# Kernel optimization log

Measured on AMD Instinct MI355X. Metric: run time of the kernel, lower is better.

Reference implementation:

```python
import jax, jax.numpy as jnp
import numpy as np

N, E, C, O, H, W, K = 32, 512, 64, 128, 64, 64, 3


def setup_inputs() -> dict:
    key = jax.random.key(0)
    k1, k2, k3, k4, k5, k6 = jax.random.split(key, 6)
    scale_w = 1.0 / np.sqrt(E)
    return {
        "embedding": jax.random.normal(k1, (N, E), dtype=jnp.float32),
        "images": jax.random.normal(k2, (N, C, H, W), dtype=jnp.float32),
        "w_weight": jax.random.uniform(k3, (O * C * K * K, E), dtype=jnp.float32, minval=-scale_w, maxval=scale_w),
        "w_bias": jax.random.uniform(k4, (O * C * K * K,), dtype=jnp.float32, minval=-scale_w, maxval=scale_w),
        "b_weight": jax.random.uniform(k5, (O, E), dtype=jnp.float32, minval=-scale_w, maxval=scale_w),
        "b_bias": jax.random.uniform(k6, (O,), dtype=jnp.float32, minval=-scale_w, maxval=scale_w),
    }


def reference(embedding, images, w_weight, w_bias, b_weight, b_bias):
    n, c, h, w = images.shape
    o = b_bias.shape[0]
    # per-sample generated filters and biases
    c1_w = embedding @ w_weight.T + w_bias          # [N, O*C*K*K]
    c1_b = embedding @ b_weight.T + b_bias          # [N, O]
    filt = c1_w.reshape(n, o, c, K, K)              # matches torch view(O, C*K*K)
    # im2col equivalent: pad then gather 3x3 shifted views -> [N,C,K,K,H,W]
    xp = jnp.pad(images, ((0, 0), (0, 0), (1, 1), (1, 1)))
    patches = jnp.stack(
        [xp[:, :, i:i + h, j:j + w] for i in range(K) for j in range(K)], axis=2
    ).reshape(n, c, K, K, h, w)
    out = jnp.einsum('nocij,ncijhw->nohw', filt, patches)
    return out + c1_b[:, :, None, None]
```

## Files before the change

kernel.cpp:

```cpp
#include <hip/hip_runtime.h>
#include <hip/hip_bf16.h>

#define N_  32
#define E_  512
#define C_  64
#define O_  128
#define H_  64
#define W_  64
#define CK9 576
#define M_  (O_*CK9)

typedef __bf16 bf16x8 __attribute__((ext_vector_type(8)));
typedef __bf16 bf16x4 __attribute__((ext_vector_type(4)));
typedef float  f32x4  __attribute__((ext_vector_type(4)));

__global__ __launch_bounds__(256) void gen_filters(
    const float* __restrict__ emb, const float* __restrict__ w_weight,
    const float* __restrict__ w_bias, __bf16* __restrict__ filt)
{
    __shared__ __align__(16) __bf16 embS[32 * 520];
    __shared__ __align__(16) __bf16 wS[128 * 40];

    int tid  = threadIdx.x;
    int wave = tid >> 6, lane = tid & 63;
    int quad = lane >> 4, l16 = lane & 15;
    int m0 = blockIdx.x * 128;

#pragma unroll
    for (int i = 0; i < 16; i++) {
        int idx = (i * 256 + tid) * 4;
        int n = idx >> 9, e = idx & 511;
        f32x4 v = *reinterpret_cast<const f32x4*>(emb + n * 512 + e);
        bf16x4 b;
        b[0] = (__bf16)v[0]; b[1] = (__bf16)v[1]; b[2] = (__bf16)v[2]; b[3] = (__bf16)v[3];
        *reinterpret_cast<bf16x4*>(&embS[n * 520 + e]) = b;
    }

    f32x4 acc[2][2];
#pragma unroll
    for (int mi = 0; mi < 2; mi++)
#pragma unroll
        for (int ni = 0; ni < 2; ni++)
            acc[mi][ni] = (f32x4){0.f, 0.f, 0.f, 0.f};

    int sub = tid & 7, rbase = tid >> 3;

    for (int kk = 0; kk < 16; kk++) {
        int k0 = kk * 32;
        __syncthreads();
#pragma unroll
        for (int q = 0; q < 4; q++) {
            int row = rbase + q * 32;
            f32x4 v = *reinterpret_cast<const f32x4*>(
                w_weight + (size_t)(m0 + row) * 512 + k0 + sub * 4);
            bf16x4 b;
            b[0] = (__bf16)v[0]; b[1] = (__bf16)v[1]; b[2] = (__bf16)v[2]; b[3] = (__bf16)v[3];
            *reinterpret_cast<bf16x4*>(&wS[row * 40 + sub * 4]) = b;
        }
        __syncthreads();

        bf16x8 a0 = *reinterpret_cast<const bf16x8*>(&wS[(wave * 32 + l16) * 40 + quad * 8]);
        bf16x8 a1 = *reinterpret_cast<const bf16x8*>(&wS[(wave * 32 + 16 + l16) * 40 + quad * 8]);
        bf16x8 b0 = *reinterpret_cast<const bf16x8*>(&embS[l16 * 520 + k0 + quad * 8]);
        bf16x8 b1 = *reinterpret_cast<const bf16x8*>(&embS[(16 + l16) * 520 + k0 + quad * 8]);
        acc[0][0] = __builtin_amdgcn_mfma_f32_16x16x32_bf16(a0, b0, acc[0][0], 0, 0, 0);
        acc[0][1] = __builtin_amdgcn_mfma_f32_16x16x32_bf16(a0, b1, acc[0][1], 0, 0, 0);
        acc[1][0] = __builtin_amdgcn_mfma_f32_16x16x32_bf16(a1, b0, acc[1][0], 0, 0, 0);
        acc[1][1] = __builtin_amdgcn_mfma_f32_16x16x32_bf16(a1, b1, acc[1][1], 0, 0, 0);
    }

#pragma unroll
    for (int mi = 0; mi < 2; mi++) {
#pragma unroll
        for (int r = 0; r < 4; r++) {
            int m = m0 + wave * 32 + mi * 16 + quad * 4 + r;
            int o = m / 576;
            int rem = m - o * 576;
            int c = rem / 9;
            int t = rem - c * 9;
            size_t base = (size_t)o * 576 + t * 64 + c;
            float bias = w_bias[m];
#pragma unroll
            for (int ni = 0; ni < 2; ni++) {
                int n = ni * 16 + l16;
                filt[(size_t)n * M_ + base] = (__bf16)(acc[mi][ni][r] + bias);
            }
        }
    }
}

__global__ __launch_bounds__(256) void gen_bias(
    const float* __restrict__ emb, const float* __restrict__ b_weight,
    const float* __restrict__ b_bias, float* __restrict__ c1b)
{
    int wid  = (blockIdx.x * 256 + threadIdx.x) >> 6;
    int lane = threadIdx.x & 63;
    int n = wid >> 7, o = wid & 127;
    const float* e = emb + (size_t)n * E_ + lane * 8;
    const float* b = b_weight + (size_t)o * E_ + lane * 8;
    f32x4 e0 = *reinterpret_cast<const f32x4*>(e);
    f32x4 e1 = *reinterpret_cast<const f32x4*>(e + 4);
    f32x4 w0 = *reinterpret_cast<const f32x4*>(b);
    f32x4 w1 = *reinterpret_cast<const f32x4*>(b + 4);
    float s = e0[0]*w0[0] + e0[1]*w0[1] + e0[2]*w0[2] + e0[3]*w0[3]
            + e1[0]*w1[0] + e1[1]*w1[1] + e1[2]*w1[2] + e1[3]*w1[3];
#pragma unroll
    for (int off = 32; off; off >>= 1) s += __shfl_xor(s, off, 64);
    if (lane == 0) c1b[wid] = s + b_bias[o];
}

__global__ __launch_bounds__(256) void conv_gemm(
    const float* __restrict__ img, const __bf16* __restrict__ filt,
    const float* __restrict__ c1b, float* __restrict__ out)
{
    __shared__ __align__(16) __bf16 slab[4 * 66 * 72];

    int tid  = threadIdx.x;
    int wave = tid >> 6, lane = tid & 63;
    int quad = lane >> 4, l16 = lane & 15;

    int blk = blockIdx.x;
    int n     = ((blk & 7) << 2) + ((blk >> 3) & 3);
    int strip = blk >> 5;

    const float* imgn = img + (size_t)n * (C_ * H_ * W_);
    const __bf16* fBase = filt + (size_t)n * M_ + (size_t)(wave * 32 + l16) * CK9 + quad * 8;

    for (int pt2 = 0; pt2 < 2; pt2++) {
        int pt = strip * 2 + pt2;
        int h0 = pt * 2;

        __syncthreads();

#pragma unroll
        for (int i = 0; i < 16; i++) {
            int idx = i * 256 + tid;
            int wq  = (idx & 15) * 4;
            int rc  = idx >> 4;
            int r = rc >> 6, c = rc & 63;
            int hh = h0 - 1 + r;
            f32x4 v = {0.f, 0.f, 0.f, 0.f};
            if ((unsigned)hh < 64u)
                v = *reinterpret_cast<const f32x4*>(imgn + ((size_t)c << 12) + (hh << 6) + wq);
            __bf16* d = &slab[(r * 66 + wq + 1) * 72 + c];
            d[0]   = (__bf16)v[0];
            d[72]  = (__bf16)v[1];
            d[144] = (__bf16)v[2];
            d[216] = (__bf16)v[3];
        }
#pragma unroll
        for (int idx = tid; idx < 512; idx += 256) {
            int cc = idx & 63, rj = idx >> 6;
            int r = rj >> 1, col = (rj & 1) * 65;
            slab[(r * 66 + col) * 72 + cc] = (__bf16)0.f;
        }
        __syncthreads();

        f32x4 acc[2][8];
#pragma unroll
        for (int mi = 0; mi < 2; mi++)
#pragma unroll
            for (int ni = 0; ni < 8; ni++)
                acc[mi][ni] = (f32x4){0.f, 0.f, 0.f, 0.f};

#pragma unroll
        for (int kh = 0; kh < 2; kh++) {
            bf16x8 aR[2][9];
#pragma unroll
            for (int mi = 0; mi < 2; mi++)
#pragma unroll
                for (int t9 = 0; t9 < 9; t9++)
                    aR[mi][t9] = *reinterpret_cast<const bf16x8*>(
                        fBase + (size_t)mi * 16 * CK9 + kh * 288 + t9 * 32);

#pragma unroll
            for (int t9 = 0; t9 < 9; t9++) {
                int kk = kh * 9 + t9;
                int k0 = kk * 32;
                int t  = k0 >> 6;
                int di = t / 3;
                int tj = t - 3 * di;
                int c0 = k0 & 32;

                bf16x8 b[8];
#pragma unroll
                for (int ni = 0; ni < 8; ni++) {
                    int lh = ni >> 2;
                    int w  = (ni & 3) * 16 + l16;
                    b[ni] = *reinterpret_cast<const bf16x8*>(
                        &slab[((lh + di) * 66 + w + tj) * 72 + c0 + quad * 8]);
                }
#pragma unroll
                for (int mi = 0; mi < 2; mi++)
#pragma unroll
                    for (int ni = 0; ni < 8; ni++)
                        acc[mi][ni] = __builtin_amdgcn_mfma_f32_16x16x32_bf16(
                            aR[mi][t9], b[ni], acc[mi][ni], 0, 0, 0);
            }
        }

#pragma unroll
        for (int mi = 0; mi < 2; mi++) {
#pragma unroll
            for (int r = 0; r < 4; r++) {
                int o = wave * 32 + mi * 16 + quad * 4 + r;
                float bias = c1b[(n << 7) + o];
                float* op = out + (((size_t)(n << 7) + o) << 12) + (pt << 7);
#pragma unroll
                for (int ni = 0; ni < 8; ni++)
                    op[(ni >> 2) * 64 + (ni & 3) * 16 + l16] = acc[mi][ni][r] + bias;
            }
        }
    }
}

extern "C" void kernel_launch(void* const* d_in, const int* in_sizes, int n_in,
                              void* d_out, int out_size, void* d_ws, size_t ws_size,
                              hipStream_t stream)
{
    (void)in_sizes; (void)n_in; (void)out_size; (void)ws_size;
    const float* emb      = (const float*)d_in[0];
    const float* images   = (const float*)d_in[1];
    const float* w_weight = (const float*)d_in[2];
    const float* w_bias   = (const float*)d_in[3];
    const float* b_weight = (const float*)d_in[4];
    const float* b_bias   = (const float*)d_in[5];
    float* out = (float*)d_out;

    __bf16* filt = (__bf16*)d_ws;
    float*  c1b  = (float*)((char*)d_ws + (size_t)N_ * M_ * 2);

    gen_filters<<<dim3(M_ / 128), dim3(256), 0, stream>>>(emb, w_weight, w_bias, filt);
    gen_bias<<<dim3(N_ * O_ / 4), dim3(256), 0, stream>>>(emb, b_weight, b_bias, c1b);
    conv_gemm<<<dim3(512), dim3(256), 0, stream>>>(images, filt, c1b, out);
}
```

Measured before the change: 330.2 us.

## Pre-pack padded bf16 image and stream slabs via global_load_lds

```diff
diff --git a/kernel.cpp b/kernel.cpp
--- a/kernel.cpp
+++ b/kernel.cpp
@@ -9,10 +9,67 @@
 #define W_  64
 #define CK9 576
 #define M_  (O_*CK9)
+#define IMGP_ROWB 9216
 
 typedef __bf16 bf16x8 __attribute__((ext_vector_type(8)));
 typedef __bf16 bf16x4 __attribute__((ext_vector_type(4)));
 typedef float  f32x4  __attribute__((ext_vector_type(4)));
+
+__device__ __forceinline__ void gload_lds16(const void* g, void* l) {
+    typedef __attribute__((address_space(1))) const void gvoid;
+    typedef __attribute__((address_space(3))) void lvoid;
+    __builtin_amdgcn_global_load_lds((gvoid*)g, (lvoid*)l, 16, 0, 0);
+}
+
+__global__ __launch_bounds__(256) void img_pack(
+    const float* __restrict__ img, __bf16* __restrict__ imgp)
+{
+    __shared__ __align__(16) __bf16 ldsT[64 * 72];
+
+    int tid = threadIdx.x;
+    int blk = blockIdx.x;
+    int n = blk / 66, hh = blk - n * 66;
+    char* dst = (char*)imgp + ((size_t)n * 66 + hh) * IMGP_ROWB;
+
+    bf16x8 zero = {(__bf16)0.f, (__bf16)0.f, (__bf16)0.f, (__bf16)0.f,
+                   (__bf16)0.f, (__bf16)0.f, (__bf16)0.f, (__bf16)0.f};
+
+    if (hh == 0 || hh == 65) {
+#pragma unroll
+        for (int j = 0; j < 3; j++) {
+            int u = j * 256 + tid;
+            if (u < 576) *reinterpret_cast<bf16x8*>(dst + u * 16) = zero;
+        }
+        return;
+    }
+
+    int h = hh - 1;
+    const float* srcn = img + (size_t)n * (C_ * H_ * W_) + h * 64;
+#pragma unroll
+    for (int i = 0; i < 4; i++) {
+        int idx = i * 256 + tid;
+        int c = idx >> 4, wq = (idx & 15) * 4;
+        f32x4 v = *reinterpret_cast<const f32x4*>(srcn + (size_t)c * 4096 + wq);
+#pragma unroll
+        for (int j = 0; j < 4; j++)
+            ldsT[(wq + j) * 72 + c] = (__bf16)v[j];
+    }
+    __syncthreads();
+
+#pragma unroll
+    for (int j = 0; j < 3; j++) {
+        int u = j * 256 + tid;
+        if (u < 576) {
+            int col = u >> 3, s = u & 7;
+            bf16x8 val = zero;
+            if (col >= 1 && col <= 64) {
+                int b = s ^ (col & 7);
+                val = *reinterpret_cast<const bf16x8*>(&ldsT[(col - 1) * 72 + b * 8]);
+            }
+            *reinterpret_cast<bf16x8*>(dst + u * 16) = val;
+        }
+    }
+}
 
 __global__ __launch_bounds__(256) void gen_filters(
     const float* __restrict__ emb, const float* __restrict__ w_weight,
@@ -78,7 +135,8 @@
             int rem = m - o * 576;
             int c = rem / 9;
             int t = rem - c * 9;
-            size_t base = (size_t)o * 576 + t * 64 + c;
+            int kp = t * 64 + c;
+            size_t base = ((size_t)(kp >> 3) << 10) + ((size_t)o << 3) + (kp & 7);
             float bias = w_bias[m];
 #pragma unroll
             for (int ni = 0; ni < 2; ni++) {
@@ -109,11 +167,11 @@
     if (lane == 0) c1b[wid] = s + b_bias[o];
 }
 
-__global__ __launch_bounds__(256) void conv_gemm(
-    const float* __restrict__ img, const __bf16* __restrict__ filt,
+__global__ __launch_bounds__(256, 2) void conv_gemm(
+    const __bf16* __restrict__ imgp, const __bf16* __restrict__ filt,
     const float* __restrict__ c1b, float* __restrict__ out)
 {
-    __shared__ __align__(16) __bf16 slab[4 * 66 * 72];
+    __shared__ __align__(16) __bf16 slab[4 * 72 * 64];
 
     int tid  = threadIdx.x;
     int wave = tid >> 6, lane = tid & 63;
@@ -123,8 +181,21 @@
     int n     = ((blk & 7) << 2) + ((blk >> 3) & 3);
     int strip = blk >> 5;
 
-    const float* imgn = img + (size_t)n * (C_ * H_ * W_);
-    const __bf16* fBase = filt + (size_t)n * M_ + (size_t)(wave * 32 + l16) * CK9 + quad * 8;
+    const __bf16* fN   = filt + (size_t)n * M_;
+    const char*   srcN = (const char*)imgp + (size_t)n * 66 * IMGP_ROWB;
+    char*         slabB = (char*)slab;
+    int oB = wave * 32 + l16;
+
+    int colA[4][3][2];
+#pragma unroll
+    for (int cb = 0; cb < 4; cb++)
+#pragma unroll
+        for (int tj = 0; tj < 3; tj++) {
+            int col = cb * 16 + l16 + tj;
+#pragma unroll
+            for (int ck = 0; ck < 2; ck++)
+                colA[cb][tj][ck] = col * 128 + (((quad + ck * 4) ^ (col & 7)) << 4);
+        }
 
     for (int pt2 = 0; pt2 < 2; pt2++) {
         int pt = strip * 2 + pt2;
@@ -132,28 +203,11 @@
 
         __syncthreads();
 
-#pragma unroll
-        for (int i = 0; i < 16; i++) {
-            int idx = i * 256 + tid;
-            int wq  = (idx & 15) * 4;
-            int rc  = idx >> 4;
-            int r = rc >> 6, c = rc & 63;
-            int hh = h0 - 1 + r;
-            f32x4 v = {0.f, 0.f, 0.f, 0.f};
-            if ((unsigned)hh < 64u)
-                v = *reinterpret_cast<const f32x4*>(imgn + ((size_t)c << 12) + (hh << 6) + wq);
-            __bf16* d = &slab[(r * 66 + wq + 1) * 72 + c];
-            d[0]   = (__bf16)v[0];
-            d[72]  = (__bf16)v[1];
-            d[144] = (__bf16)v[2];
-            d[216] = (__bf16)v[3];
-        }
-#pragma unroll
-        for (int idx = tid; idx < 512; idx += 256) {
-            int cc = idx & 63, rj = idx >> 6;
-            int r = rj >> 1, col = (rj & 1) * 65;
-            slab[(r * 66 + col) * 72 + cc] = (__bf16)0.f;
-        }
+        const char* src = srcN + (size_t)h0 * IMGP_ROWB;
+#pragma unroll
+        for (int j = 0; j < 9; j++)
+            gload_lds16(src + (j * 256 + tid) * 16,
+                        slabB + (j * 256 + wave * 64) * 16);
         __syncthreads();
 
         f32x4 acc[2][8];
@@ -171,24 +225,22 @@
 #pragma unroll
                 for (int t9 = 0; t9 < 9; t9++)
                     aR[mi][t9] = *reinterpret_cast<const bf16x8*>(
-                        fBase + (size_t)mi * 16 * CK9 + kh * 288 + t9 * 32);
+                        fN + (((kh * 36 + t9 * 4 + quad) << 10) + ((oB + mi * 16) << 3)));
 
 #pragma unroll
             for (int t9 = 0; t9 < 9; t9++) {
                 int kk = kh * 9 + t9;
-                int k0 = kk * 32;
-                int t  = k0 >> 6;
+                int t  = kk >> 1;
+                int ck = kk & 1;
                 int di = t / 3;
                 int tj = t - 3 * di;
-                int c0 = k0 & 32;
 
                 bf16x8 b[8];
 #pragma unroll
                 for (int ni = 0; ni < 8; ni++) {
-                    int lh = ni >> 2;
-                    int w  = (ni & 3) * 16 + l16;
+                    int row = (ni >> 2) + di;
                     b[ni] = *reinterpret_cast<const bf16x8*>(
-                        &slab[((lh + di) * 66 + w + tj) * 72 + c0 + quad * 8]);
+                        slabB + row * IMGP_ROWB + colA[ni & 3][tj][ck]);
                 }
 #pragma unroll
                 for (int mi = 0; mi < 2; mi++)
@@ -229,8 +281,10 @@
 
     __bf16* filt = (__bf16*)d_ws;
     float*  c1b  = (float*)((char*)d_ws + (size_t)N_ * M_ * 2);
-
+    __bf16* imgp = (__bf16*)((char*)d_ws + (size_t)N_ * M_ * 2 + 16384);
+
+    img_pack<<<dim3(N_ * 66), dim3(256), 0, stream>>>(images, imgp);
     gen_filters<<<dim3(M_ / 128), dim3(256), 0, stream>>>(emb, w_weight, w_bias, filt);
     gen_bias<<<dim3(N_ * O_ / 4), dim3(256), 0, stream>>>(emb, b_weight, b_bias, c1b);
-    conv_gemm<<<dim3(512), dim3(256), 0, stream>>>(images, filt, c1b, out);
-}
+    conv_gemm<<<dim3(512), dim3(256), 0, stream>>>(imgp, filt, c1b, out);
+}
```

After: 333.0 us. Within noise of the previous version (+0.8%).
